# Kernel optimization log

Measured on AMD Instinct MI355X. Metric: run time of the kernel, lower is better.

The kernel has to match this reference:

```python
import jax, jax.numpy as jnp
import numpy as np

N, E, D, L = 50000, 250000, 300, 5
ATOM_V, BOND_V = 128, 16
BN_EPS = 1e-5


def setup_inputs() -> dict:
    key = jax.random.key(0)
    ks = jax.random.split(key, 16)
    inp = {
        'x': jax.random.randint(ks[0], (N, 9), 0, ATOM_V),
        'edge_index': jax.random.randint(ks[1], (2, E), 0, N),
        'edge_attr': jax.random.randint(ks[2], (E, 3), 0, BOND_V),
        # learned parameters
        'atom_emb': jax.random.normal(ks[3], (9, ATOM_V, D), jnp.float32) * 0.02,
        'bond_emb': jax.random.normal(ks[4], (L, 3, BOND_V, D), jnp.float32) * 0.02,
        'eps': jnp.zeros((L,), jnp.float32),
        'W1': jax.random.normal(ks[5], (L, D, 2 * D), jnp.float32) / np.sqrt(D),
        'b1': jnp.zeros((L, 2 * D), jnp.float32),
        'g1': jnp.ones((L, 2 * D), jnp.float32),
        'be1': jnp.zeros((L, 2 * D), jnp.float32),
        'W2': jax.random.normal(ks[6], (L, 2 * D, D), jnp.float32) / np.sqrt(2 * D),
        'b2': jnp.zeros((L, D), jnp.float32),
        'gamma': jnp.ones((L, D), jnp.float32),
        'beta': jnp.zeros((L, D), jnp.float32),
    }
    return inp


def _bn(h, g, b):
    m = h.mean(0)
    v = h.var(0)
    return (h - m) * jax.lax.rsqrt(v + BN_EPS) * g + b


def reference(x, edge_index, edge_attr, atom_emb, bond_emb, eps, W1, b1, g1, be1, W2, b2, gamma, beta):
    src, dst = edge_index[0], edge_index[1]
    # AtomEncoder: sum of per-column embeddings -> [N, D]
    h = atom_emb[jnp.arange(9)[:, None], x.T].sum(0)
    for l in range(L):
        # BondEncoder for this layer -> [E, D]
        e = bond_emb[l][jnp.arange(3)[:, None], edge_attr.T].sum(0)
        # GIN: gather -> relu message -> scatter-add
        msg = jax.nn.relu(h[src] + e)
        agg = jax.ops.segment_sum(msg, dst, num_segments=N)
        z = (1.0 + eps[l]) * h + agg
        # MLP: Linear -> BN -> ReLU -> Linear
        z = jax.nn.relu(_bn(z @ W1[l] + b1[l], g1[l], be1[l])) @ W2[l] + b2[l]
        # outer BatchNorm
        h = _bn(z, gamma[l], beta[l])
        if l < L - 1:
            h = jax.nn.relu(h)
    return h  # JK='last'
```

## Files before the change

### kernel.cpp

```cpp
#include <hip/hip_runtime.h>

#define N_NODES 50000
#define N_EDGES 250000
#define DIM 300
#define DIM2 600
#define NL 5
#define MPAD 50048
#define KP1 320
#define KP2 608
#define NP1 640
#define NP2 384
#define SCAN_BLOCKS 196
#define CT_STRIDE 136

typedef __attribute__((ext_vector_type(8))) _Float16 half8;
typedef __attribute__((ext_vector_type(2))) _Float16 half2v;
typedef __attribute__((ext_vector_type(8))) short short8;
typedef __attribute__((ext_vector_type(4))) float f32x4;
typedef unsigned short ushort;
typedef unsigned int uint;

#define AS1 __attribute__((address_space(1)))
#define AS3 __attribute__((address_space(3)))

#define BARRIER() do { \
    asm volatile("" ::: "memory"); \
    __builtin_amdgcn_s_barrier(); \
    asm volatile("" ::: "memory"); \
} while (0)

static __device__ __forceinline__ ushort f2h(float f) {
    _Float16 h = (_Float16)f;
    return __builtin_bit_cast(ushort, h);
}
static __device__ __forceinline__ float h2f(ushort s) {
    return (float)__builtin_bit_cast(_Float16, s);
}
static __device__ __forceinline__ uint pk2(float a, float b) {
    return (uint)f2h(a) | ((uint)f2h(b) << 16);
}
static __device__ __forceinline__ half2v u2h2(uint u) {
    return __builtin_bit_cast(half2v, u);
}

static __device__ __forceinline__ int xcd_swizzle(int o, int nwg) {
    int q = nwg >> 3, r = nwg & 7;
    int xcd = o & 7, idx = o >> 3;
    return (xcd < r ? xcd * (q + 1) : r * (q + 1) + (xcd - r) * q) + idx;
}

__global__ void atom_enc(const int* __restrict__ x, const float* __restrict__ emb,
                         ushort* __restrict__ h) {
    int idx = blockIdx.x * blockDim.x + threadIdx.x;
    const int PAIRS = DIM / 2;
    if (idx >= N_NODES * PAIRS) return;
    int n = idx / PAIRS, p = idx - n * PAIRS;
    const int* xr = x + n * 9;
    float s0 = 0.f, s1 = 0.f;
#pragma unroll
    for (int i = 0; i < 9; i++) {
        const float2 v = *(const float2*)(emb + (size_t)(i * 128 + xr[i]) * DIM + 2 * p);
        s0 += v.x; s1 += v.y;
    }
    ((uint*)h)[idx] = pk2(s0, s1);
}

__global__ void deg_count(const int* __restrict__ ei, int* __restrict__ deg) {
    int e = blockIdx.x * blockDim.x + threadIdx.x;
    if (e < N_EDGES) atomicAdd(&deg[ei[N_EDGES + e]], 1);
}

__global__ void block_sums(const int* __restrict__ deg, int* __restrict__ bsum) {
    __shared__ int red[256];
    int tid = threadIdx.x;
    int node = blockIdx.x * 256 + tid;
    red[tid] = (node < N_NODES) ? deg[node] : 0;
    __syncthreads();
    for (int off = 128; off > 0; off >>= 1) {
        if (tid < off) red[tid] += red[tid + off];
        __syncthreads();
    }
    if (tid == 0) bsum[blockIdx.x] = red[0];
}

__global__ void scan_bsums(int* __restrict__ bsum) {
    __shared__ int s[256];
    int tid = threadIdx.x;
    int orig = (tid < SCAN_BLOCKS) ? bsum[tid] : 0;
    s[tid] = orig;
    __syncthreads();
    for (int off = 1; off < 256; off <<= 1) {
        int v = (tid >= off) ? s[tid - off] : 0;
        __syncthreads();
        s[tid] += v;
        __syncthreads();
    }
    if (tid < SCAN_BLOCKS) bsum[tid] = s[tid] - orig;
}

__global__ void write_rowstart(const int* __restrict__ deg, const int* __restrict__ bsum,
                               int* __restrict__ rowstart, int* __restrict__ cursor) {
    __shared__ int s[256];
    int tid = threadIdx.x;
    int node = blockIdx.x * 256 + tid;
    int d = (node < N_NODES) ? deg[node] : 0;
    s[tid] = d;
    __syncthreads();
    for (int off = 1; off < 256; off <<= 1) {
        int v = (tid >= off) ? s[tid - off] : 0;
        __syncthreads();
        s[tid] += v;
        __syncthreads();
    }
    int excl = s[tid] - d + bsum[blockIdx.x];
    if (node < N_NODES) {
        rowstart[node] = excl;
        cursor[node] = excl;
    }
    if (blockIdx.x == 0 && tid == 0) rowstart[N_NODES] = N_EDGES;
}

__global__ void csr_fill(const int* __restrict__ ei, const int* __restrict__ ea,
                         int* __restrict__ cursor, int2* __restrict__ epack) {
    int e = blockIdx.x * blockDim.x + threadIdx.x;
    if (e < N_EDGES) {
        int d = ei[N_EDGES + e];
        int slot = atomicAdd(&cursor[d], 1);
        int attr = ea[3 * e] | (ea[3 * e + 1] << 8) | (ea[3 * e + 2] << 16);
        epack[slot] = make_int2(ei[e], attr);
    }
}

__global__ void bond_conv(const float* __restrict__ bond, ushort* __restrict__ bondh) {
    int idx = blockIdx.x * blockDim.x + threadIdx.x;
    if (idx >= 48 * (DIM / 2)) return;
    float2 v = *(const float2*)(bond + 2 * idx);
    ((uint*)bondh)[idx] = pk2(v.x, v.y);
}

__global__ void init_bn(float* __restrict__ scale, float* __restrict__ shift) {
    int i = blockIdx.x * blockDim.x + threadIdx.x;
    if (i < DIM) { scale[i] = 1.f; shift[i] = 0.f; }
}

__launch_bounds__(256)
__global__ void agg_combine(const int* __restrict__ rowstart, const int2* __restrict__ epack,
                            const ushort* __restrict__ bondh, const ushort* __restrict__ h,
                            const float* __restrict__ scale, const float* __restrict__ shift,
                            int relu, const float* __restrict__ epsp, int layer,
                            ushort* __restrict__ A1) {
    int node = blockIdx.x * 4 + (threadIdx.x >> 6);
    int lane = threadIdx.x & 63;
    if (node >= MPAD) return;
    uint* row32 = (uint*)(A1 + (size_t)node * KP1);
    if (node >= N_NODES) {
        for (int i = lane; i < KP1 / 2; i += 64) row32[i] = 0;
        return;
    }
    const int PAIRS = DIM / 2;
    float2 scf[3], shf[3];
    half2v sch[3], shh[3];
#pragma unroll
    for (int i = 0; i < 3; i++) {
        int p = lane + 64 * i;
        scf[i] = make_float2(0.f, 0.f);
        shf[i] = make_float2(0.f, 0.f);
        if (p < PAIRS) {
            scf[i] = *(const float2*)(scale + 2 * p);
            shf[i] = *(const float2*)(shift + 2 * p);
        }
        sch[i] = half2v{(_Float16)scf[i].x, (_Float16)scf[i].y};
        shh[i] = half2v{(_Float16)shf[i].x, (_Float16)shf[i].y};
    }
    float epsv = 1.0f + epsp[layer];
    const uint* hd = (const uint*)(h + (size_t)node * DIM);
    float ax[3], ay[3];
#pragma unroll
    for (int i = 0; i < 3; i++) {
        int p = lane + 64 * i;
        ax[i] = 0.f; ay[i] = 0.f;
        if (p < PAIRS) {
            uint u = hd[p];
            float vx = h2f((ushort)(u & 0xffffu)) * scf[i].x + shf[i].x;
            float vy = h2f((ushort)(u >> 16)) * scf[i].y + shf[i].y;
            if (relu) { vx = fmaxf(vx, 0.f); vy = fmaxf(vy, 0.f); }
            ax[i] = epsv * vx; ay[i] = epsv * vy;
        }
    }

    auto edge_contrib = [&](int2 pk) {
        const uint* hs = (const uint*)(h + (size_t)pk.x * DIM);
        int a0 = pk.y & 0xff, a1v = (pk.y >> 8) & 0xff, a2 = (pk.y >> 16) & 0xff;
        const uint* t0 = (const uint*)(bondh + a0 * DIM);
        const uint* t1 = (const uint*)(bondh + (16 + a1v) * DIM);
        const uint* t2 = (const uint*)(bondh + (32 + a2) * DIM);
        const half2v z = {};
#pragma unroll
        for (int i = 0; i < 3; i++) {
            int p = lane + 64 * i;
            if (p < PAIRS) {
                half2v hv = u2h2(hs[p]) * sch[i] + shh[i];
                if (relu) hv = __builtin_elementwise_max(hv, z);
                half2v m = hv + u2h2(t0[p]) + u2h2(t1[p]) + u2h2(t2[p]);
                m = __builtin_elementwise_max(m, z);
                ax[i] += (float)m.x;
                ay[i] += (float)m.y;
            }
        }
    };

    int e0 = rowstart[node], e1 = rowstart[node + 1];
    int t = e0;
    for (; t + 1 < e1; t += 2) {
        int2 p0 = epack[t];
        int2 p1 = epack[t + 1];
        edge_contrib(p0);
        edge_contrib(p1);
    }
    if (t < e1) edge_contrib(epack[t]);

#pragma unroll
    for (int i = 0; i < 3; i++) {
        int p = lane + 64 * i;
        if (p < KP1 / 2) row32[p] = (p < PAIRS) ? pk2(ax[i], ay[i]) : 0u;
    }
}

__global__ void wt_conv(const float* __restrict__ W, ushort* __restrict__ Wt,
                        int K, int Nc, int KP, int NP) {
    int idx = blockIdx.x * blockDim.x + threadIdx.x;
    if (idx >= KP * NP) return;
    int k = idx / NP, n = idx - k * NP;
    ushort v = 0;
    if (k < K && n < Nc) v = f2h(W[(size_t)k * Nc + n]);
    Wt[(size_t)n * KP + k] = v;
}

__global__ void wt_conv2(const float* __restrict__ W, const float* __restrict__ scale,
                         ushort* __restrict__ Wt) {
    int idx = blockIdx.x * blockDim.x + threadIdx.x;
    if (idx >= KP2 * NP2) return;
    int k = idx / NP2, n = idx - k * NP2;
    ushort v = 0;
    if (k < DIM2 && n < DIM) v = f2h(scale[k] * W[(size_t)k * DIM + n]);
    Wt[(size_t)n * KP2 + k] = v;
}

__launch_bounds__(256, 4)
__global__ void gemm_mfma(const ushort* __restrict__ A, const ushort* __restrict__ Wt,
                          const float* __restrict__ bias, ushort* __restrict__ Cout,
                          int M, int KP, int Nc, int strideC, int ntiles,
                          float* __restrict__ csum, float* __restrict__ csq) {
    __shared__ ushort smem[16384];
    __shared__ float s_sum[128], s_sq[128];

    int tid = threadIdx.x;
    int w = tid >> 6, lane = tid & 63;
    int quad = lane >> 4, lr = lane & 15;
    int wm = w >> 1, wn = w & 1;
    int wg = xcd_swizzle(blockIdx.x, gridDim.x);
    int m0 = (wg / ntiles) * 128;
    int n0 = (wg % ntiles) * 128;

    if (tid < 128) { s_sum[tid] = 0.f; s_sq[tid] = 0.f; }

    const int kchunk = ((lane & 3) ^ ((lane >> 3) & 3)) * 8;
    const int grow = lane >> 2;
    const ushort* Abase = A + (size_t)m0 * KP + kchunk;
    const ushort* Bbase = Wt + (size_t)n0 * KP + kchunk;
    const int xq = (quad ^ ((lr >> 1) & 3)) * 8;

    auto stage = [&](int k0, int buf) {
        ushort* dA = smem + buf * 8192;
#pragma unroll
        for (int c = w; c < 8; c += 4)
            __builtin_amdgcn_global_load_lds((const AS1 void*)(Abase + (size_t)(16 * c + grow) * KP + k0),
                                             (AS3 void*)(dA + c * 512), 16, 0, 0);
#pragma unroll
        for (int c = w; c < 8; c += 4)
            __builtin_amdgcn_global_load_lds((const AS1 void*)(Bbase + (size_t)(16 * c + grow) * KP + k0),
                                             (AS3 void*)(dA + 4096 + c * 512), 16, 0, 0);
    };

    f32x4 acc[4][4] = {};
    const int nk = KP >> 5;

    stage(0, 0);
    stage(32, 1);
    asm volatile("s_waitcnt vmcnt(4)" ::: "memory");
    BARRIER();

    for (int t = 0; t < nk; ++t) {
        const ushort* As = smem + (t & 1) * 8192;
        const ushort* Bs = As + 4096;
        half8 a[4], b[4];
#pragma unroll
        for (int mf = 0; mf < 4; mf++)
            a[mf] = __builtin_bit_cast(half8, *(const short8*)(As + (64 * wm + 16 * mf + lr) * 32 + xq));
#pragma unroll
        for (int nf = 0; nf < 4; nf++)
            b[nf] = __builtin_bit_cast(half8, *(const short8*)(Bs + (64 * wn + 16 * nf + lr) * 32 + xq));
        asm volatile("s_waitcnt lgkmcnt(0)" ::: "memory");
        BARRIER();

        if (t + 2 < nk) stage((t + 2) << 5, t & 1);

        __builtin_amdgcn_s_setprio(1);
#pragma unroll
        for (int mf = 0; mf < 4; mf++)
#pragma unroll
            for (int nf = 0; nf < 4; nf++)
                acc[mf][nf] = __builtin_amdgcn_mfma_f32_16x16x32_f16(a[mf], b[nf], acc[mf][nf], 0, 0, 0);
        __builtin_amdgcn_s_setprio(0);

        if (t + 2 < nk)       { asm volatile("s_waitcnt vmcnt(4)" ::: "memory"); }
        else if (t + 1 < nk)  { asm volatile("s_waitcnt vmcnt(0)" ::: "memory"); }
        BARRIER();
    }

#pragma unroll
    for (int half = 0; half < 2; half++) {
        if (wm == half) {
#pragma unroll
            for (int nf = 0; nf < 4; nf++) {
                int lcol = 64 * wn + 16 * nf + lr;
                int gn = n0 + lcol;
                float bv = (gn < Nc) ? bias[gn] : 0.f;
                float ps = 0.f, pq = 0.f;
#pragma unroll
                for (int mf = 0; mf < 4; mf++) {
#pragma unroll
                    for (int r = 0; r < 4; r++) {
                        int lrow = 16 * mf + quad * 4 + r;
                        float v = acc[mf][nf][r] + bv;
                        smem[lrow * CT_STRIDE + lcol] = f2h(v);
                        if (m0 + 64 * half + lrow < M && gn < Nc) { ps += v; pq += v * v; }
                    }
                }
                if (gn < Nc) {
                    atomicAdd(&s_sum[lcol], ps);
                    atomicAdd(&s_sq[lcol], pq);
                }
            }
        }
        __syncthreads();
#pragma unroll
        for (int it = 0; it < 4; it++) {
            int idx = tid + it * 256;
            int row = idx >> 4, ch = idx & 15;
            int gcol = n0 + ch * 8;
            if (gcol < Nc) {
                *(short8*)(Cout + (size_t)(m0 + 64 * half + row) * strideC + gcol) =
                    *(const short8*)(smem + row * CT_STRIDE + ch * 8);
            }
        }
        __syncthreads();
    }

    if (tid < 128) {
        int gn = n0 + tid;
        if (gn < Nc) {
            atomicAdd(&csum[gn], s_sum[tid]);
            atomicAdd(&csq[gn], s_sq[tid]);
        }
    }
}

__launch_bounds__(256, 4)
__global__ void gemm2_fused(const ushort* __restrict__ yh, const ushort* __restrict__ Wt,
                            const ushort* __restrict__ t1h, const float* __restrict__ bias,
                            ushort* __restrict__ hout,
                            float* __restrict__ csum, float* __restrict__ csq) {
    __shared__ ushort smem[20480];
    __shared__ ushort s_t[KP2];
    __shared__ float s_sum[128], s_sq[128];

    int tid = threadIdx.x;
    int w = tid >> 6, lane = tid & 63;
    int quad = lane >> 4, lr = lane & 15;
    int wm = w >> 1, wn = w & 1;
    int wg = xcd_swizzle(blockIdx.x, gridDim.x);
    int m0 = (wg / 3) * 128;
    int n0 = (wg % 3) * 128;

    int r0 = tid >> 2;
    int q = tid & 3;
    int cc = q * 8;
    const int aslot = (q ^ ((r0 >> 1) & 3)) * 8;

    const int kchunk = ((lane & 3) ^ ((lane >> 3) & 3)) * 8;
    const int grow = lane >> 2;
    const ushort* Bbase = Wt + (size_t)n0 * KP2 + kchunk;
    const int xq = (quad ^ ((lr >> 1) & 3)) * 8;

    const ushort* yrow0 = yh + (size_t)(m0 + r0) * DIM2 + cc;
    const ushort* yrow1 = yh + (size_t)(m0 + r0 + 64) * DIM2 + cc;

    auto stageB = [&](int k0, int buf) {
        ushort* dB = smem + 8192 + buf * 4096;
#pragma unroll
        for (int c = w; c < 8; c += 4)
            __builtin_amdgcn_global_load_lds((const AS1 void*)(Bbase + (size_t)(16 * c + grow) * KP2 + k0),
                                             (AS3 void*)(dB + c * 512), 16, 0, 0);
    };

    if (tid < 128) { s_sum[tid] = 0.f; s_sq[tid] = 0.f; }

    for (int i = tid; i < KP2 / 2; i += 256) ((uint*)s_t)[i] = ((const uint*)t1h)[i];
    half8 y0 = *(const half8*)(yrow0);
    half8 y1 = *(const half8*)(yrow1);
    stageB(0, 0);
    stageB(32, 1);
    asm volatile("s_waitcnt lgkmcnt(0)" ::: "memory");
    BARRIER();
    {
        half8 z = {};
        half8 tt = *(const half8*)(s_t + cc);
        half8 a0 = __builtin_elementwise_max(y0 + tt, z);
        half8 a1 = __builtin_elementwise_max(y1 + tt, z);
        *(short8*)(smem + r0 * 32 + aslot) = __builtin_bit_cast(short8, a0);
        *(short8*)(smem + (r0 + 64) * 32 + aslot) = __builtin_bit_cast(short8, a1);
    }
    asm volatile("s_waitcnt vmcnt(2) lgkmcnt(0)" ::: "memory");
    BARRIER();

    f32x4 acc[4][4] = {};
    const int nk = KP2 >> 5;

    for (int t = 0; t < nk; ++t) {
        half8 yn0 = {}, yn1 = {};
        int coln = ((t + 1) << 5) + cc;
        if (t + 1 < nk && coln < DIM2) {
            yn0 = *(const half8*)(yrow0 + ((t + 1) << 5));
            yn1 = *(const half8*)(yrow1 + ((t + 1) << 5));
        }
        if (t + 2 < nk) stageB((t + 2) << 5, (t + 2) % 3);

        const ushort* As = smem + (t & 1) * 4096;
        const ushort* Bs = smem + 8192 + (t % 3) * 4096;
        half8 a[4], b[4];
#pragma unroll
        for (int mf = 0; mf < 4; mf++)
            a[mf] = __builtin_bit_cast(half8, *(const short8*)(As + (64 * wm + 16 * mf + lr) * 32 + xq));
#pragma unroll
        for (int nf = 0; nf < 4; nf++)
            b[nf] = __builtin_bit_cast(half8, *(const short8*)(Bs + (64 * wn + 16 * nf + lr) * 32 + xq));
        asm volatile("s_waitcnt lgkmcnt(0)" ::: "memory");
        __builtin_amdgcn_sched_barrier(0);

        __builtin_amdgcn_s_setprio(1);
#pragma unroll
        for (int mf = 0; mf < 4; mf++)
#pragma unroll
            for (int nf = 0; nf < 4; nf++)
                acc[mf][nf] = __builtin_amdgcn_mfma_f32_16x16x32_f16(a[mf], b[nf], acc[mf][nf], 0, 0, 0);
        __builtin_amdgcn_s_setprio(0);

        if (t + 1 < nk) {
            half8 z = {};
            half8 tt = *(const half8*)(s_t + coln);
            half8 a0 = __builtin_elementwise_max(yn0 + tt, z);
            half8 a1 = __builtin_elementwise_max(yn1 + tt, z);
            ushort* Anx = smem + ((t + 1) & 1) * 4096;
            *(short8*)(Anx + r0 * 32 + aslot) = __builtin_bit_cast(short8, a0);
            *(short8*)(Anx + (r0 + 64) * 32 + aslot) = __builtin_bit_cast(short8, a1);
        }
        asm volatile("s_waitcnt lgkmcnt(0)" ::: "memory");
        BARRIER();
    }

#pragma unroll
    for (int half = 0; half < 2; half++) {
        if (wm == half) {
#pragma unroll
            for (int nf = 0; nf < 4; nf++) {
                int lcol = 64 * wn + 16 * nf + lr;
                int gn = n0 + lcol;
                float bv = (gn < DIM) ? bias[gn] : 0.f;
                float ps = 0.f, pq = 0.f;
#pragma unroll
                for (int mf = 0; mf < 4; mf++) {
#pragma unroll
                    for (int r = 0; r < 4; r++) {
                        int lrow = 16 * mf + quad * 4 + r;
                        float v = acc[mf][nf][r] + bv;
                        smem[lrow * CT_STRIDE + lcol] = f2h(v);
                        if (m0 + 64 * half + lrow < N_NODES && gn < DIM) { ps += v; pq += v * v; }
                    }
                }
                if (gn < DIM) {
                    atomicAdd(&s_sum[lcol], ps);
                    atomicAdd(&s_sq[lcol], pq);
                }
            }
        }
        __syncthreads();
#pragma unroll
        for (int it = 0; it < 8; it++) {
            int idx = tid + it * 256;
            int row = idx >> 5, ch = idx & 31;
            int gm = m0 + 64 * half + row, gcol = n0 + ch * 4;
            if (gm < N_NODES && gcol < DIM) {
                *(uint2*)(hout + (size_t)gm * DIM + gcol) =
                    *(const uint2*)(smem + row * CT_STRIDE + ch * 4);
            }
        }
        __syncthreads();
    }

    if (tid < 128) {
        int gn = n0 + tid;
        if (gn < DIM) {
            atomicAdd(&csum[gn], s_sum[tid]);
            atomicAdd(&csq[gn], s_sq[tid]);
        }
    }
}

__global__ void bn_finalize(const float* __restrict__ sum, const float* __restrict__ sq,
                            const float* __restrict__ g, const float* __restrict__ b,
                            float* __restrict__ scale, float* __restrict__ shift,
                            ushort* __restrict__ th, int n, int npad) {
    int i = blockIdx.x * blockDim.x + threadIdx.x;
    if (i >= n) {
        if (th && i < npad) th[i] = 0;
        return;
    }
    const float invN = 1.0f / (float)N_NODES;
    float m = sum[i] * invN;
    float v = sq[i] * invN - m * m;
    float inv = rsqrtf(v + 1e-5f);
    float sc = g[i] * inv;
    scale[i] = sc;
    shift[i] = b[i] - m * sc;
    if (th) th[i] = f2h((b[i] - m * sc) / sc);
}

__global__ void bn_apply_out(const ushort* __restrict__ h, const float* __restrict__ scale,
                             const float* __restrict__ shift, float* __restrict__ out) {
    int idx = blockIdx.x * blockDim.x + threadIdx.x;
    const int PAIRS = DIM / 2;
    if (idx >= N_NODES * PAIRS) return;
    int p = idx % PAIRS;
    uint u = ((const uint*)h)[idx];
    float2 sc = *(const float2*)(scale + 2 * p);
    float2 sh = *(const float2*)(shift + 2 * p);
    float2 o;
    o.x = h2f((ushort)(u & 0xffffu)) * sc.x + sh.x;
    o.y = h2f((ushort)(u >> 16)) * sc.y + sh.y;
    *(float2*)(out + 2 * idx) = o;
}

extern "C" void kernel_launch(void* const* d_in, const int* in_sizes, int n_in,
                              void* d_out, int out_size, void* d_ws, size_t ws_size,
                              hipStream_t stream) {
    const int* x = (const int*)d_in[0];
    const int* ei = (const int*)d_in[1];
    const int* ea = (const int*)d_in[2];
    const float* atom_emb = (const float*)d_in[3];
    const float* bond_emb = (const float*)d_in[4];
    const float* eps = (const float*)d_in[5];
    const float* W1 = (const float*)d_in[6];
    const float* b1 = (const float*)d_in[7];
    const float* g1 = (const float*)d_in[8];
    const float* be1 = (const float*)d_in[9];
    const float* W2 = (const float*)d_in[10];
    const float* b2 = (const float*)d_in[11];
    const float* gamma = (const float*)d_in[12];
    const float* beta = (const float*)d_in[13];
    float* out = (float*)d_out;

    float* ws = (float*)d_ws;
    ushort* h    = (ushort*)ws;
    ushort* A1h  = (ushort*)(ws + 7500000);
    ushort* yh   = (ushort*)(ws + 15507680);
    ushort* Wt1  = (ushort*)(ws + 30522080);
    ushort* Wt2  = (ushort*)(ws + 30624480);
    ushort* bondh = (ushort*)(ws + 30741216);
    float* stats = ws + 30748416;
    ushort* t1h  = (ushort*)(ws + 30752016);
    int* rowstart = (int*)(ws + 30752320);
    int* deg      = rowstart + 50001;
    int* cursor   = deg + 50000;
    int2* epack   = (int2*)(cursor + 50000 + 1);
    int* bsum     = (int*)(epack + 250000);

    float* sum1 = stats;
    float* sq1  = stats + 600;
    float* sum2 = stats + 1200;
    float* sq2  = stats + 1500;
    float* scale1 = stats + 1800;
    float* shift1 = stats + 2400;
    float* scale2 = stats + 3000;
    float* shift2 = stats + 3300;

    const int PAIRS_N = N_NODES * (DIM / 2);

    hipMemsetAsync(deg, 0, 50000 * sizeof(int), stream);
    deg_count<<<(N_EDGES + 255) / 256, 256, 0, stream>>>(ei, deg);
    block_sums<<<SCAN_BLOCKS, 256, 0, stream>>>(deg, bsum);
    scan_bsums<<<1, 256, 0, stream>>>(bsum);
    write_rowstart<<<SCAN_BLOCKS, 256, 0, stream>>>(deg, bsum, rowstart, cursor);
    csr_fill<<<(N_EDGES + 255) / 256, 256, 0, stream>>>(ei, ea, cursor, epack);

    atom_enc<<<(PAIRS_N + 255) / 256, 256, 0, stream>>>(x, atom_emb, h);
    init_bn<<<(DIM + 255) / 256, 256, 0, stream>>>(scale2, shift2);

    for (int l = 0; l < NL; ++l) {
        hipMemsetAsync(stats, 0, 1800 * sizeof(float), stream);

        bond_conv<<<(48 * (DIM / 2) + 255) / 256, 256, 0, stream>>>(
            bond_emb + (size_t)l * 3 * 16 * DIM, bondh);

        agg_combine<<<(MPAD + 3) / 4, 256, 0, stream>>>(rowstart, epack, bondh,
                                                        h, scale2, shift2, (l > 0) ? 1 : 0,
                                                        eps, l, A1h);

        wt_conv<<<(KP1 * NP1 + 255) / 256, 256, 0, stream>>>(W1 + (size_t)l * DIM * DIM2, Wt1,
                                                             DIM, DIM2, KP1, NP1);

        gemm_mfma<<<(MPAD / 128) * (NP1 / 128), 256, 0, stream>>>(
            A1h, Wt1, b1 + l * DIM2, yh, N_NODES, KP1, DIM2, DIM2, NP1 / 128, sum1, sq1);

        bn_finalize<<<(KP2 + 255) / 256, 256, 0, stream>>>(sum1, sq1, g1 + l * DIM2,
                                                           be1 + l * DIM2, scale1, shift1,
                                                           t1h, DIM2, KP2);

        wt_conv2<<<(KP2 * NP2 + 255) / 256, 256, 0, stream>>>(W2 + (size_t)l * DIM2 * DIM,
                                                              scale1, Wt2);

        gemm2_fused<<<(MPAD / 128) * (NP2 / 128), 256, 0, stream>>>(
            yh, Wt2, t1h, b2 + l * DIM, h, sum2, sq2);

        bn_finalize<<<(DIM + 255) / 256, 256, 0, stream>>>(sum2, sq2, gamma + l * DIM,
                                                           beta + l * DIM, scale2, shift2,
                                                           nullptr, DIM, DIM);
    }

    bn_apply_out<<<(PAIRS_N + 255) / 256, 256, 0, stream>>>(h, scale2, shift2, out);
}
```

Measured before the change: 1.090 ms.

## Enlarge GEMM M-tile to 256 rows and stage yh via async LDS loads

Both MFMA GEMMs move from 128x128 to 256x128 tiles, so each warp now holds 8x4 accumulator fragments and every B tile is reused across twice as many rows. The second GEMM drops its register-path A prefetch and applies the BN-shift plus ReLU in registers after loading raw yh through global_load_lds, so yh is now written padded to stride KP2. The workspace layout and row padding (MPAD2) change to match. The cost is higher register pressure and lower occupancy (launch bounds relaxed), and fewer blocks in the grid.

```diff
diff --git a/kernel.cpp b/kernel.cpp
--- a/kernel.cpp
+++ b/kernel.cpp
@@ -5,7 +5,7 @@
 #define DIM 300
 #define DIM2 600
 #define NL 5
-#define MPAD 50048
+#define MPAD2 50176
 #define KP1 320
 #define KP2 608
 #define NP1 640
@@ -151,7 +151,7 @@
                             ushort* __restrict__ A1) {
     int node = blockIdx.x * 4 + (threadIdx.x >> 6);
     int lane = threadIdx.x & 63;
-    if (node >= MPAD) return;
+    if (node >= MPAD2) return;
     uint* row32 = (uint*)(A1 + (size_t)node * KP1);
     if (node >= N_NODES) {
         for (int i = lane; i < KP1 / 2; i += 64) row32[i] = 0;
@@ -246,12 +246,12 @@
     Wt[(size_t)n * KP2 + k] = v;
 }
 
-__launch_bounds__(256, 4)
+__launch_bounds__(256)
 __global__ void gemm_mfma(const ushort* __restrict__ A, const ushort* __restrict__ Wt,
                           const float* __restrict__ bias, ushort* __restrict__ Cout,
                           int M, int KP, int Nc, int strideC, int ntiles,
                           float* __restrict__ csum, float* __restrict__ csq) {
-    __shared__ ushort smem[16384];
+    __shared__ ushort smem[24576];
     __shared__ float s_sum[128], s_sq[128];
 
     int tid = threadIdx.x;
@@ -259,7 +259,7 @@
     int quad = lane >> 4, lr = lane & 15;
     int wm = w >> 1, wn = w & 1;
     int wg = xcd_swizzle(blockIdx.x, gridDim.x);
-    int m0 = (wg / ntiles) * 128;
+    int m0 = (wg / ntiles) * 256;
     int n0 = (wg % ntiles) * 128;
 
     if (tid < 128) { s_sum[tid] = 0.f; s_sq[tid] = 0.f; }
@@ -272,31 +272,32 @@
 
     auto stage = [&](int k0, int buf) {
         ushort* dA = smem + buf * 8192;
-#pragma unroll
-        for (int c = w; c < 8; c += 4)
+        ushort* dB = smem + 16384 + buf * 4096;
+#pragma unroll
+        for (int c = w; c < 16; c += 4)
             __builtin_amdgcn_global_load_lds((const AS1 void*)(Abase + (size_t)(16 * c + grow) * KP + k0),
                                              (AS3 void*)(dA + c * 512), 16, 0, 0);
 #pragma unroll
         for (int c = w; c < 8; c += 4)
             __builtin_amdgcn_global_load_lds((const AS1 void*)(Bbase + (size_t)(16 * c + grow) * KP + k0),
-                                             (AS3 void*)(dA + 4096 + c * 512), 16, 0, 0);
+                                             (AS3 void*)(dB + c * 512), 16, 0, 0);
     };
 
-    f32x4 acc[4][4] = {};
+    f32x4 acc[8][4] = {};
     const int nk = KP >> 5;
 
     stage(0, 0);
     stage(32, 1);
-    asm volatile("s_waitcnt vmcnt(4)" ::: "memory");
+    asm volatile("s_waitcnt vmcnt(6)" ::: "memory");
     BARRIER();
 
     for (int t = 0; t < nk; ++t) {
         const ushort* As = smem + (t & 1) * 8192;
-        const ushort* Bs = As + 4096;
-        half8 a[4], b[4];
-#pragma unroll
-        for (int mf = 0; mf < 4; mf++)
-            a[mf] = __builtin_bit_cast(half8, *(const short8*)(As + (64 * wm + 16 * mf + lr) * 32 + xq));
+        const ushort* Bs = smem + 16384 + (t & 1) * 4096;
+        half8 a[8], b[4];
+#pragma unroll
+        for (int mf = 0; mf < 8; mf++)
+            a[mf] = __builtin_bit_cast(half8, *(const short8*)(As + (128 * wm + 16 * mf + lr) * 32 + xq));
 #pragma unroll
         for (int nf = 0; nf < 4; nf++)
             b[nf] = __builtin_bit_cast(half8, *(const short8*)(Bs + (64 * wn + 16 * nf + lr) * 32 + xq));
@@ -307,20 +308,20 @@
 
         __builtin_amdgcn_s_setprio(1);
 #pragma unroll
-        for (int mf = 0; mf < 4; mf++)
+        for (int mf = 0; mf < 8; mf++)
 #pragma unroll
             for (int nf = 0; nf < 4; nf++)
                 acc[mf][nf] = __builtin_amdgcn_mfma_f32_16x16x32_f16(a[mf], b[nf], acc[mf][nf], 0, 0, 0);
         __builtin_amdgcn_s_setprio(0);
 
-        if (t + 2 < nk)       { asm volatile("s_waitcnt vmcnt(4)" ::: "memory"); }
+        if (t + 2 < nk)       { asm volatile("s_waitcnt vmcnt(6)" ::: "memory"); }
         else if (t + 1 < nk)  { asm volatile("s_waitcnt vmcnt(0)" ::: "memory"); }
         BARRIER();
     }
 
 #pragma unroll
-    for (int half = 0; half < 2; half++) {
-        if (wm == half) {
+    for (int band = 0; band < 4; band++) {
+        if (wm == (band >> 1)) {
 #pragma unroll
             for (int nf = 0; nf < 4; nf++) {
                 int lcol = 64 * wn + 16 * nf + lr;
@@ -328,13 +329,14 @@
                 float bv = (gn < Nc) ? bias[gn] : 0.f;
                 float ps = 0.f, pq = 0.f;
 #pragma unroll
-                for (int mf = 0; mf < 4; mf++) {
+                for (int mf4 = 0; mf4 < 4; mf4++) {
+                    int mf = (band & 1) * 4 + mf4;
 #pragma unroll
                     for (int r = 0; r < 4; r++) {
-                        int lrow = 16 * mf + quad * 4 + r;
+                        int lrow = 16 * mf4 + quad * 4 + r;
                         float v = acc[mf][nf][r] + bv;
                         smem[lrow * CT_STRIDE + lcol] = f2h(v);
-                        if (m0 + 64 * half + lrow < M && gn < Nc) { ps += v; pq += v * v; }
+                        if (m0 + 64 * band + lrow < M && gn < Nc) { ps += v; pq += v * v; }
                     }
                 }
                 if (gn < Nc) {
@@ -349,8 +351,8 @@
             int idx = tid + it * 256;
             int row = idx >> 4, ch = idx & 15;
             int gcol = n0 + ch * 8;
-            if (gcol < Nc) {
-                *(short8*)(Cout + (size_t)(m0 + 64 * half + row) * strideC + gcol) =
+            if (gcol < strideC) {
+                *(short8*)(Cout + (size_t)(m0 + 64 * band + row) * strideC + gcol) =
                     *(const short8*)(smem + row * CT_STRIDE + ch * 8);
             }
         }
@@ -366,12 +368,12 @@
     }
 }
 
-__launch_bounds__(256, 4)
+__launch_bounds__(256)
 __global__ void gemm2_fused(const ushort* __restrict__ yh, const ushort* __restrict__ Wt,
                             const ushort* __restrict__ t1h, const float* __restrict__ bias,
                             ushort* __restrict__ hout,
                             float* __restrict__ csum, float* __restrict__ csq) {
-    __shared__ ushort smem[20480];
+    __shared__ ushort smem[24576];
     __shared__ ushort s_t[KP2];
     __shared__ float s_sum[128], s_sq[128];
 
@@ -380,98 +382,79 @@
     int quad = lane >> 4, lr = lane & 15;
     int wm = w >> 1, wn = w & 1;
     int wg = xcd_swizzle(blockIdx.x, gridDim.x);
-    int m0 = (wg / 3) * 128;
+    int m0 = (wg / 3) * 256;
     int n0 = (wg % 3) * 128;
 
-    int r0 = tid >> 2;
-    int q = tid & 3;
-    int cc = q * 8;
-    const int aslot = (q ^ ((r0 >> 1) & 3)) * 8;
+    if (tid < 128) { s_sum[tid] = 0.f; s_sq[tid] = 0.f; }
 
     const int kchunk = ((lane & 3) ^ ((lane >> 3) & 3)) * 8;
     const int grow = lane >> 2;
+    const ushort* Abase = yh + (size_t)m0 * KP2 + kchunk;
     const ushort* Bbase = Wt + (size_t)n0 * KP2 + kchunk;
     const int xq = (quad ^ ((lr >> 1) & 3)) * 8;
 
-    const ushort* yrow0 = yh + (size_t)(m0 + r0) * DIM2 + cc;
-    const ushort* yrow1 = yh + (size_t)(m0 + r0 + 64) * DIM2 + cc;
-
-    auto stageB = [&](int k0, int buf) {
-        ushort* dB = smem + 8192 + buf * 4096;
+    auto stage = [&](int k0, int buf) {
+        ushort* dA = smem + buf * 8192;
+        ushort* dB = smem + 16384 + buf * 4096;
+#pragma unroll
+        for (int c = w; c < 16; c += 4)
+            __builtin_amdgcn_global_load_lds((const AS1 void*)(Abase + (size_t)(16 * c + grow) * KP2 + k0),
+                                             (AS3 void*)(dA + c * 512), 16, 0, 0);
 #pragma unroll
         for (int c = w; c < 8; c += 4)
             __builtin_amdgcn_global_load_lds((const AS1 void*)(Bbase + (size_t)(16 * c + grow) * KP2 + k0),
                                              (AS3 void*)(dB + c * 512), 16, 0, 0);
     };
 
-    if (tid < 128) { s_sum[tid] = 0.f; s_sq[tid] = 0.f; }
-
     for (int i = tid; i < KP2 / 2; i += 256) ((uint*)s_t)[i] = ((const uint*)t1h)[i];
-    half8 y0 = *(const half8*)(yrow0);
-    half8 y1 = *(const half8*)(yrow1);
-    stageB(0, 0);
-    stageB(32, 1);
-    asm volatile("s_waitcnt lgkmcnt(0)" ::: "memory");
+    asm volatile("s_waitcnt vmcnt(0) lgkmcnt(0)" ::: "memory");
+    stage(0, 0);
+    stage(32, 1);
+    asm volatile("s_waitcnt vmcnt(6)" ::: "memory");
     BARRIER();
-    {
-        half8 z = {};
-        half8 tt = *(const half8*)(s_t + cc);
-        half8 a0 = __builtin_elementwise_max(y0 + tt, z);
-        half8 a1 = __builtin_elementwise_max(y1 + tt, z);
-        *(short8*)(smem + r0 * 32 + aslot) = __builtin_bit_cast(short8, a0);
-        *(short8*)(smem + (r0 + 64) * 32 + aslot) = __builtin_bit_cast(short8, a1);
-    }
-    asm volatile("s_waitcnt vmcnt(2) lgkmcnt(0)" ::: "memory");
-    BARRIER();
-
-    f32x4 acc[4][4] = {};
+
+    f32x4 acc[8][4] = {};
     const int nk = KP2 >> 5;
 
     for (int t = 0; t < nk; ++t) {
-        half8 yn0 = {}, yn1 = {};
-        int coln = ((t + 1) << 5) + cc;
-        if (t + 1 < nk && coln < DIM2) {
-            yn0 = *(const half8*)(yrow0 + ((t + 1) << 5));
-            yn1 = *(const half8*)(yrow1 + ((t + 1) << 5));
-        }
-        if (t + 2 < nk) stageB((t + 2) << 5, (t + 2) % 3);
-
-        const ushort* As = smem + (t & 1) * 4096;
-        const ushort* Bs = smem + 8192 + (t % 3) * 4096;
-        half8 a[4], b[4];
-#pragma unroll
-        for (int mf = 0; mf < 4; mf++)
-            a[mf] = __builtin_bit_cast(half8, *(const short8*)(As + (64 * wm + 16 * mf + lr) * 32 + xq));
+        int k0 = t << 5;
+        const ushort* As = smem + (t & 1) * 8192;
+        const ushort* Bs = smem + 16384 + (t & 1) * 4096;
+        half8 a[8], b[4];
+        half8 t8 = *(const half8*)(s_t + k0 + quad * 8);
+#pragma unroll
+        for (int mf = 0; mf < 8; mf++)
+            a[mf] = __builtin_bit_cast(half8, *(const short8*)(As + (128 * wm + 16 * mf + lr) * 32 + xq));
 #pragma unroll
         for (int nf = 0; nf < 4; nf++)
             b[nf] = __builtin_bit_cast(half8, *(const short8*)(Bs + (64 * wn + 16 * nf + lr) * 32 + xq));
         asm volatile("s_waitcnt lgkmcnt(0)" ::: "memory");
-        __builtin_amdgcn_sched_barrier(0);
+        BARRIER();
+
+        if (t + 2 < nk) stage((t + 2) << 5, t & 1);
 
         __builtin_amdgcn_s_setprio(1);
-#pragma unroll
-        for (int mf = 0; mf < 4; mf++)
+        {
+            half8 z = {};
+#pragma unroll
+            for (int mf = 0; mf < 8; mf++)
+                a[mf] = __builtin_elementwise_max(a[mf] + t8, z);
+        }
+#pragma unroll
+        for (int mf = 0; mf < 8; mf++)
 #pragma unroll
             for (int nf = 0; nf < 4; nf++)
                 acc[mf][nf] = __builtin_amdgcn_mfma_f32_16x16x32_f16(a[mf], b[nf], acc[mf][nf], 0, 0, 0);
         __builtin_amdgcn_s_setprio(0);
 
-        if (t + 1 < nk) {
-            half8 z = {};
-            half8 tt = *(const half8*)(s_t + coln);
-            half8 a0 = __builtin_elementwise_max(yn0 + tt, z);
-            half8 a1 = __builtin_elementwise_max(yn1 + tt, z);
-            ushort* Anx = smem + ((t + 1) & 1) * 4096;
-            *(short8*)(Anx + r0 * 32 + aslot) = __builtin_bit_cast(short8, a0);
-            *(short8*)(Anx + (r0 + 64) * 32 + aslot) = __builtin_bit_cast(short8, a1);
-        }
-        asm volatile("s_waitcnt lgkmcnt(0)" ::: "memory");
+        if (t + 2 < nk)       { asm volatile("s_waitcnt vmcnt(6)" ::: "memory"); }
+        else if (t + 1 < nk)  { asm volatile("s_waitcnt vmcnt(0)" ::: "memory"); }
         BARRIER();
     }
 
 #pragma unroll
-    for (int half = 0; half < 2; half++) {
-        if (wm == half) {
+    for (int band = 0; band < 4; band++) {
+        if (wm == (band >> 1)) {
 #pragma unroll
             for (int nf = 0; nf < 4; nf++) {
                 int lcol = 64 * wn + 16 * nf + lr;
@@ -479,13 +462,14 @@
                 float bv = (gn < DIM) ? bias[gn] : 0.f;
                 float ps = 0.f, pq = 0.f;
 #pragma unroll
-                for (int mf = 0; mf < 4; mf++) {
+                for (int mf4 = 0; mf4 < 4; mf4++) {
+                    int mf = (band & 1) * 4 + mf4;
 #pragma unroll
                     for (int r = 0; r < 4; r++) {
-                        int lrow = 16 * mf + quad * 4 + r;
+                        int lrow = 16 * mf4 + quad * 4 + r;
                         float v = acc[mf][nf][r] + bv;
                         smem[lrow * CT_STRIDE + lcol] = f2h(v);
-                        if (m0 + 64 * half + lrow < N_NODES && gn < DIM) { ps += v; pq += v * v; }
+                        if (m0 + 64 * band + lrow < N_NODES && gn < DIM) { ps += v; pq += v * v; }
                     }
                 }
                 if (gn < DIM) {
@@ -499,7 +483,7 @@
         for (int it = 0; it < 8; it++) {
             int idx = tid + it * 256;
             int row = idx >> 5, ch = idx & 31;
-            int gm = m0 + 64 * half + row, gcol = n0 + ch * 4;
+            int gm = m0 + 64 * band + row, gcol = n0 + ch * 4;
             if (gm < N_NODES && gcol < DIM) {
                 *(uint2*)(hout + (size_t)gm * DIM + gcol) =
                     *(const uint2*)(smem + row * CT_STRIDE + ch * 4);
@@ -573,13 +557,13 @@
     float* ws = (float*)d_ws;
     ushort* h    = (ushort*)ws;
     ushort* A1h  = (ushort*)(ws + 7500000);
-    ushort* yh   = (ushort*)(ws + 15507680);
-    ushort* Wt1  = (ushort*)(ws + 30522080);
-    ushort* Wt2  = (ushort*)(ws + 30624480);
-    ushort* bondh = (ushort*)(ws + 30741216);
-    float* stats = ws + 30748416;
-    ushort* t1h  = (ushort*)(ws + 30752016);
-    int* rowstart = (int*)(ws + 30752320);
+    ushort* yh   = (ushort*)(ws + 15528160);
+    ushort* Wt1  = (ushort*)(ws + 30781664);
+    ushort* Wt2  = (ushort*)(ws + 30884064);
+    ushort* bondh = (ushort*)(ws + 31000800);
+    float* stats = ws + 31008000;
+    ushort* t1h  = (ushort*)(ws + 31011600);
+    int* rowstart = (int*)(ws + 31011904);
     int* deg      = rowstart + 50001;
     int* cursor   = deg + 50000;
     int2* epack   = (int2*)(cursor + 50000 + 1);
@@ -612,15 +596,15 @@
         bond_conv<<<(48 * (DIM / 2) + 255) / 256, 256, 0, stream>>>(
             bond_emb + (size_t)l * 3 * 16 * DIM, bondh);
 
-        agg_combine<<<(MPAD + 3) / 4, 256, 0, stream>>>(rowstart, epack, bondh,
-                                                        h, scale2, shift2, (l > 0) ? 1 : 0,
-                                                        eps, l, A1h);
+        agg_combine<<<(MPAD2 + 3) / 4, 256, 0, stream>>>(rowstart, epack, bondh,
+                                                         h, scale2, shift2, (l > 0) ? 1 : 0,
+                                                         eps, l, A1h);
 
         wt_conv<<<(KP1 * NP1 + 255) / 256, 256, 0, stream>>>(W1 + (size_t)l * DIM * DIM2, Wt1,
                                                              DIM, DIM2, KP1, NP1);
 
-        gemm_mfma<<<(MPAD / 128) * (NP1 / 128), 256, 0, stream>>>(
-            A1h, Wt1, b1 + l * DIM2, yh, N_NODES, KP1, DIM2, DIM2, NP1 / 128, sum1, sq1);
+        gemm_mfma<<<(MPAD2 / 256) * (NP1 / 128), 256, 0, stream>>>(
+            A1h, Wt1, b1 + l * DIM2, yh, N_NODES, KP1, DIM2, KP2, NP1 / 128, sum1, sq1);
 
         bn_finalize<<<(KP2 + 255) / 256, 256, 0, stream>>>(sum1, sq1, g1 + l * DIM2,
                                                            be1 + l * DIM2, scale1, shift1,
@@ -629,7 +613,7 @@
         wt_conv2<<<(KP2 * NP2 + 255) / 256, 256, 0, stream>>>(W2 + (size_t)l * DIM2 * DIM,
                                                               scale1, Wt2);
 
-        gemm2_fused<<<(MPAD / 128) * (NP2 / 128), 256, 0, stream>>>(
+        gemm2_fused<<<(MPAD2 / 256) * (NP2 / 128), 256, 0, stream>>>(
             yh, Wt2, t1h, b2 + l * DIM, h, sum2, sq2);
 
         bn_finalize<<<(DIM + 255) / 256, 256, 0, stream>>>(sum2, sq2, gamma + l * DIM,
```

New measurement: 1.337 ms. 22.6% more time.

## Use triple-buffered LDS pipeline and direct-to-LDS A loads in both GEMMs

Applied to the files above, without the earlier changes.

Both GEMM kernels now use a three-slot LDS ring, issuing the stage-ahead global_load_lds before the fragment reads, which removes one barrier per K step. The second GEMM stops staging A through registers with an in-flight relu/shift and instead loads the padded yh directly into LDS, applying the shift-and-relu on the fragments just before the MFMAs. To allow this, the first GEMM writes yh with a padded row stride (KP2) including the pad columns, and the workspace layout is shifted to fit. This costs more LDS per block, and the launch bounds drop the min-blocks hint, which may change occupancy.

```diff
diff --git a/kernel.cpp b/kernel.cpp
--- a/kernel.cpp
+++ b/kernel.cpp
@@ -246,12 +246,12 @@
     Wt[(size_t)n * KP2 + k] = v;
 }
 
-__launch_bounds__(256, 4)
+__launch_bounds__(256)
 __global__ void gemm_mfma(const ushort* __restrict__ A, const ushort* __restrict__ Wt,
                           const float* __restrict__ bias, ushort* __restrict__ Cout,
                           int M, int KP, int Nc, int strideC, int ntiles,
                           float* __restrict__ csum, float* __restrict__ csq) {
-    __shared__ ushort smem[16384];
+    __shared__ ushort smem[24576];
     __shared__ float s_sum[128], s_sq[128];
 
     int tid = threadIdx.x;
@@ -271,7 +271,8 @@
     const int xq = (quad ^ ((lr >> 1) & 3)) * 8;
 
     auto stage = [&](int k0, int buf) {
-        ushort* dA = smem + buf * 8192;
+        ushort* dA = smem + buf * 4096;
+        ushort* dB = smem + 12288 + buf * 4096;
 #pragma unroll
         for (int c = w; c < 8; c += 4)
             __builtin_amdgcn_global_load_lds((const AS1 void*)(Abase + (size_t)(16 * c + grow) * KP + k0),
@@ -279,7 +280,7 @@
 #pragma unroll
         for (int c = w; c < 8; c += 4)
             __builtin_amdgcn_global_load_lds((const AS1 void*)(Bbase + (size_t)(16 * c + grow) * KP + k0),
-                                             (AS3 void*)(dA + 4096 + c * 512), 16, 0, 0);
+                                             (AS3 void*)(dB + c * 512), 16, 0, 0);
     };
 
     f32x4 acc[4][4] = {};
@@ -290,9 +291,13 @@
     asm volatile("s_waitcnt vmcnt(4)" ::: "memory");
     BARRIER();
 
+    int cur = 0;
     for (int t = 0; t < nk; ++t) {
-        const ushort* As = smem + (t & 1) * 8192;
-        const ushort* Bs = As + 4096;
+        int s2 = cur + 2; if (s2 >= 3) s2 -= 3;
+        if (t + 2 < nk) stage((t + 2) << 5, s2);
+
+        const ushort* As = smem + cur * 4096;
+        const ushort* Bs = smem + 12288 + cur * 4096;
         half8 a[4], b[4];
 #pragma unroll
         for (int mf = 0; mf < 4; mf++)
@@ -301,9 +306,6 @@
         for (int nf = 0; nf < 4; nf++)
             b[nf] = __builtin_bit_cast(half8, *(const short8*)(Bs + (64 * wn + 16 * nf + lr) * 32 + xq));
         asm volatile("s_waitcnt lgkmcnt(0)" ::: "memory");
-        BARRIER();
-
-        if (t + 2 < nk) stage((t + 2) << 5, t & 1);
 
         __builtin_amdgcn_s_setprio(1);
 #pragma unroll
@@ -316,6 +318,8 @@
         if (t + 2 < nk)       { asm volatile("s_waitcnt vmcnt(4)" ::: "memory"); }
         else if (t + 1 < nk)  { asm volatile("s_waitcnt vmcnt(0)" ::: "memory"); }
         BARRIER();
+
+        cur = (cur + 1 == 3) ? 0 : cur + 1;
     }
 
 #pragma unroll
@@ -349,7 +353,7 @@
             int idx = tid + it * 256;
             int row = idx >> 4, ch = idx & 15;
             int gcol = n0 + ch * 8;
-            if (gcol < Nc) {
+            if (gcol < strideC) {
                 *(short8*)(Cout + (size_t)(m0 + 64 * half + row) * strideC + gcol) =
                     *(const short8*)(smem + row * CT_STRIDE + ch * 8);
             }
@@ -366,12 +370,12 @@
     }
 }
 
-__launch_bounds__(256, 4)
+__launch_bounds__(256)
 __global__ void gemm2_fused(const ushort* __restrict__ yh, const ushort* __restrict__ Wt,
                             const ushort* __restrict__ t1h, const float* __restrict__ bias,
                             ushort* __restrict__ hout,
                             float* __restrict__ csum, float* __restrict__ csq) {
-    __shared__ ushort smem[20480];
+    __shared__ ushort smem[24576];
     __shared__ ushort s_t[KP2];
     __shared__ float s_sum[128], s_sq[128];
 
@@ -383,62 +387,46 @@
     int m0 = (wg / 3) * 128;
     int n0 = (wg % 3) * 128;
 
-    int r0 = tid >> 2;
-    int q = tid & 3;
-    int cc = q * 8;
-    const int aslot = (q ^ ((r0 >> 1) & 3)) * 8;
+    if (tid < 128) { s_sum[tid] = 0.f; s_sq[tid] = 0.f; }
 
     const int kchunk = ((lane & 3) ^ ((lane >> 3) & 3)) * 8;
     const int grow = lane >> 2;
+    const ushort* Abase = yh + (size_t)m0 * KP2 + kchunk;
     const ushort* Bbase = Wt + (size_t)n0 * KP2 + kchunk;
     const int xq = (quad ^ ((lr >> 1) & 3)) * 8;
 
-    const ushort* yrow0 = yh + (size_t)(m0 + r0) * DIM2 + cc;
-    const ushort* yrow1 = yh + (size_t)(m0 + r0 + 64) * DIM2 + cc;
-
-    auto stageB = [&](int k0, int buf) {
-        ushort* dB = smem + 8192 + buf * 4096;
+    auto stage = [&](int k0, int buf) {
+        ushort* dA = smem + buf * 4096;
+        ushort* dB = smem + 12288 + buf * 4096;
+#pragma unroll
+        for (int c = w; c < 8; c += 4)
+            __builtin_amdgcn_global_load_lds((const AS1 void*)(Abase + (size_t)(16 * c + grow) * KP2 + k0),
+                                             (AS3 void*)(dA + c * 512), 16, 0, 0);
 #pragma unroll
         for (int c = w; c < 8; c += 4)
             __builtin_amdgcn_global_load_lds((const AS1 void*)(Bbase + (size_t)(16 * c + grow) * KP2 + k0),
                                              (AS3 void*)(dB + c * 512), 16, 0, 0);
     };
 
-    if (tid < 128) { s_sum[tid] = 0.f; s_sq[tid] = 0.f; }
-
     for (int i = tid; i < KP2 / 2; i += 256) ((uint*)s_t)[i] = ((const uint*)t1h)[i];
-    half8 y0 = *(const half8*)(yrow0);
-    half8 y1 = *(const half8*)(yrow1);
-    stageB(0, 0);
-    stageB(32, 1);
-    asm volatile("s_waitcnt lgkmcnt(0)" ::: "memory");
-    BARRIER();
-    {
-        half8 z = {};
-        half8 tt = *(const half8*)(s_t + cc);
-        half8 a0 = __builtin_elementwise_max(y0 + tt, z);
-        half8 a1 = __builtin_elementwise_max(y1 + tt, z);
-        *(short8*)(smem + r0 * 32 + aslot) = __builtin_bit_cast(short8, a0);
-        *(short8*)(smem + (r0 + 64) * 32 + aslot) = __builtin_bit_cast(short8, a1);
-    }
-    asm volatile("s_waitcnt vmcnt(2) lgkmcnt(0)" ::: "memory");
+    asm volatile("s_waitcnt vmcnt(0) lgkmcnt(0)" ::: "memory");
+    stage(0, 0);
+    stage(32, 1);
+    asm volatile("s_waitcnt vmcnt(4)" ::: "memory");
     BARRIER();
 
     f32x4 acc[4][4] = {};
     const int nk = KP2 >> 5;
 
+    int cur = 0;
     for (int t = 0; t < nk; ++t) {
-        half8 yn0 = {}, yn1 = {};
-        int coln = ((t + 1) << 5) + cc;
-        if (t + 1 < nk && coln < DIM2) {
-            yn0 = *(const half8*)(yrow0 + ((t + 1) << 5));
-            yn1 = *(const half8*)(yrow1 + ((t + 1) << 5));
-        }
-        if (t + 2 < nk) stageB((t + 2) << 5, (t + 2) % 3);
-
-        const ushort* As = smem + (t & 1) * 4096;
-        const ushort* Bs = smem + 8192 + (t % 3) * 4096;
+        int s2 = cur + 2; if (s2 >= 3) s2 -= 3;
+        if (t + 2 < nk) stage((t + 2) << 5, s2);
+
+        const ushort* As = smem + cur * 4096;
+        const ushort* Bs = smem + 12288 + cur * 4096;
         half8 a[4], b[4];
+        half8 t8 = *(const half8*)(s_t + (t << 5) + quad * 8);
 #pragma unroll
         for (int mf = 0; mf < 4; mf++)
             a[mf] = __builtin_bit_cast(half8, *(const short8*)(As + (64 * wm + 16 * mf + lr) * 32 + xq));
@@ -446,9 +434,14 @@
         for (int nf = 0; nf < 4; nf++)
             b[nf] = __builtin_bit_cast(half8, *(const short8*)(Bs + (64 * wn + 16 * nf + lr) * 32 + xq));
         asm volatile("s_waitcnt lgkmcnt(0)" ::: "memory");
-        __builtin_amdgcn_sched_barrier(0);
 
         __builtin_amdgcn_s_setprio(1);
+        {
+            half8 z = {};
+#pragma unroll
+            for (int mf = 0; mf < 4; mf++)
+                a[mf] = __builtin_elementwise_max(a[mf] + t8, z);
+        }
 #pragma unroll
         for (int mf = 0; mf < 4; mf++)
 #pragma unroll
@@ -456,17 +449,11 @@
                 acc[mf][nf] = __builtin_amdgcn_mfma_f32_16x16x32_f16(a[mf], b[nf], acc[mf][nf], 0, 0, 0);
         __builtin_amdgcn_s_setprio(0);
 
-        if (t + 1 < nk) {
-            half8 z = {};
-            half8 tt = *(const half8*)(s_t + coln);
-            half8 a0 = __builtin_elementwise_max(yn0 + tt, z);
-            half8 a1 = __builtin_elementwise_max(yn1 + tt, z);
-            ushort* Anx = smem + ((t + 1) & 1) * 4096;
-            *(short8*)(Anx + r0 * 32 + aslot) = __builtin_bit_cast(short8, a0);
-            *(short8*)(Anx + (r0 + 64) * 32 + aslot) = __builtin_bit_cast(short8, a1);
-        }
-        asm volatile("s_waitcnt lgkmcnt(0)" ::: "memory");
+        if (t + 2 < nk)       { asm volatile("s_waitcnt vmcnt(4)" ::: "memory"); }
+        else if (t + 1 < nk)  { asm volatile("s_waitcnt vmcnt(0)" ::: "memory"); }
         BARRIER();
+
+        cur = (cur + 1 == 3) ? 0 : cur + 1;
     }
 
 #pragma unroll
@@ -574,12 +561,12 @@
     ushort* h    = (ushort*)ws;
     ushort* A1h  = (ushort*)(ws + 7500000);
     ushort* yh   = (ushort*)(ws + 15507680);
-    ushort* Wt1  = (ushort*)(ws + 30522080);
-    ushort* Wt2  = (ushort*)(ws + 30624480);
-    ushort* bondh = (ushort*)(ws + 30741216);
-    float* stats = ws + 30748416;
-    ushort* t1h  = (ushort*)(ws + 30752016);
-    int* rowstart = (int*)(ws + 30752320);
+    ushort* Wt1  = (ushort*)(ws + 30722272);
+    ushort* Wt2  = (ushort*)(ws + 30824672);
+    ushort* bondh = (ushort*)(ws + 30941408);
+    float* stats = ws + 30948608;
+    ushort* t1h  = (ushort*)(ws + 30952208);
+    int* rowstart = (int*)(ws + 30952512);
     int* deg      = rowstart + 50001;
     int* cursor   = deg + 50000;
     int2* epack   = (int2*)(cursor + 50000 + 1);
@@ -620,7 +607,7 @@
                                                              DIM, DIM2, KP1, NP1);
 
         gemm_mfma<<<(MPAD / 128) * (NP1 / 128), 256, 0, stream>>>(
-            A1h, Wt1, b1 + l * DIM2, yh, N_NODES, KP1, DIM2, DIM2, NP1 / 128, sum1, sq1);
+            A1h, Wt1, b1 + l * DIM2, yh, N_NODES, KP1, DIM2, KP2, NP1 / 128, sum1, sq1);
 
         bn_finalize<<<(KP2 + 255) / 256, 256, 0, stream>>>(sum1, sq1, g1 + l * DIM2,
                                                            be1 + l * DIM2, scale1, shift1,
```

Result: slower. 1.130 ms (+3.6%).
